# Performance work log

Hardware: AMD Instinct MI355X
Metric: run time of the kernel (lower is better)

The kernel has to match this reference:

```python
import jax, jax.numpy as jnp
import numpy as np

N = 50000          # nodes
E = 400000         # edges (before self loops)
F_IN = 256         # num_node_features
H = 4              # heads
C = 64             # hidden_channels
G = 128            # graphs in batch
NEG_SLOPE = 0.2    # PyG GATConv default


def gat_conv(x, W, att_src, att_dst, bias, src, dst):
    """PyG GATConv (concat=True, add_self_loops=True). x:[N,Fin] -> [N,H*C]."""
    h = (x @ W).reshape(N, H, C)                       # [N,H,C]
    a_src = jnp.einsum('nhc,hc->nh', h, att_src)       # [N,H]
    a_dst = jnp.einsum('nhc,hc->nh', h, att_dst)       # [N,H]
    # add self loops
    loop = jnp.arange(N, dtype=src.dtype)
    s = jnp.concatenate([src, loop])                   # [E+N]
    d = jnp.concatenate([dst, loop])                   # [E+N]
    logits = jax.nn.leaky_relu(a_src[s] + a_dst[d], NEG_SLOPE)  # [E+N,H]
    # segment softmax over destination nodes
    m = jax.ops.segment_max(logits, d, num_segments=N)           # [N,H]
    m = jnp.where(jnp.isneginf(m), 0.0, m)
    ex = jnp.exp(logits - m[d])                                  # [E+N,H]
    denom = jax.ops.segment_sum(ex, d, num_segments=N)           # [N,H]
    alpha = ex / (denom[d] + 1e-16)                              # [E+N,H]
    # weighted scatter-add of source features
    msg = alpha[:, :, None] * h[s]                               # [E+N,H,C]
    out = jax.ops.segment_sum(msg, d, num_segments=N)            # [N,H,C]
    return out.reshape(N, H * C) + bias


def setup_inputs() -> dict:
    key = jax.random.key(0)
    ks = jax.random.split(key, 16)
    HC = H * C
    x = jax.random.normal(ks[0], (N, F_IN), dtype=jnp.float32)
    edge_index = jax.random.randint(ks[1], (2, E), 0, N, dtype=jnp.int32)
    batch = jnp.sort(jax.random.randint(ks[2], (N,), 0, G, dtype=jnp.int32))
    def glorot(k, shape):
        fan = shape[0] + shape[-1]
        return jax.random.uniform(k, shape, jnp.float32, -1.0, 1.0) * np.sqrt(6.0 / fan)
    return {
        'x': x, 'edge_index': edge_index, 'batch': batch,
        'W1': glorot(ks[3], (F_IN, HC)),
        'att_src1': glorot(ks[4], (H, C)), 'att_dst1': glorot(ks[5], (H, C)),
        'b1': jnp.zeros((HC,), jnp.float32),
        'W2': glorot(ks[6], (HC, HC)),
        'att_src2': glorot(ks[7], (H, C)), 'att_dst2': glorot(ks[8], (H, C)),
        'b2': jnp.zeros((HC,), jnp.float32),
        'lin1_w': glorot(ks[9], (HC, HC // 2)), 'lin1_b': jnp.zeros((HC // 2,), jnp.float32),
        'lin2_w': glorot(ks[10], (HC // 2, 2)), 'lin2_b': jnp.zeros((2,), jnp.float32),
    }


def reference(x, edge_index, batch, W1, att_src1, att_dst1, b1,
              W2, att_src2, att_dst2, b2, lin1_w, lin1_b, lin2_w, lin2_b):
    src, dst = edge_index[0], edge_index[1]
    # dropout layers are identity in eval mode
    h = gat_conv(x, W1, att_src1, att_dst1, b1, src, dst)
    h = jax.nn.elu(h)
    h = gat_conv(h, W2, att_src2, att_dst2, b2, src, dst)
    h = jax.nn.elu(h)
    pooled = jax.ops.segment_max(h, batch, num_segments=G)   # [G, H*C]
    pooled = jnp.where(jnp.isneginf(pooled), 0.0, pooled)    # guard empty graphs
    z = pooled @ lin1_w + lin1_b
    z = z @ lin2_w + lin2_b
    return z  # [G, num_classes]
```

## Files before the change

kernel.cpp:

```cpp
#include <hip/hip_runtime.h>
#include <math.h>

#define LRELU_SLOPE 0.2f
#define NEG_INF __int_as_float(0xff800000)

typedef float f32x4 __attribute__((ext_vector_type(4)));
typedef _Float16 f16x8 __attribute__((ext_vector_type(8)));
typedef _Float16 f16x2 __attribute__((ext_vector_type(2)));
typedef unsigned short us8 __attribute__((ext_vector_type(8)));

__device__ __forceinline__ void atomicMaxF(float* addr, float v) {
  if (v >= 0.f) atomicMax((int*)addr, __float_as_int(v));
  else atomicMin((unsigned int*)addr, (unsigned int)__float_as_int(v));
}

__device__ __forceinline__ unsigned short f2h(float f) {
  _Float16 h = (_Float16)f;
  return __builtin_bit_cast(unsigned short, h);
}
__device__ __forceinline__ float h2f(unsigned short u) {
  return (float)__builtin_bit_cast(_Float16, u);
}
__device__ __forceinline__ float2 up2(unsigned int u) {
  f16x2 h = __builtin_bit_cast(f16x2, u);
  return make_float2((float)h.x, (float)h.y);
}

__device__ __forceinline__ void async_copy16(const unsigned short* g, unsigned short* l) {
  __builtin_amdgcn_global_load_lds(
      (const __attribute__((address_space(1))) void*)g,
      (__attribute__((address_space(3))) void*)l, 16, 0, 0);
}

__global__ void conv_w(const float* __restrict__ W1, const float* __restrict__ W2,
                       unsigned short* __restrict__ t1, unsigned short* __restrict__ t2) {
  const float* W = blockIdx.y ? W2 : W1;
  unsigned short* t = blockIdx.y ? t2 : t1;
  int k = blockIdx.x, n = threadIdx.x;
  t[n * 256 + k] = f2h(W[k * 256 + n]);
}

__global__ __launch_bounds__(256) void conv_x(
    const float* __restrict__ x, unsigned short* __restrict__ xo, int total) {
  int base = (blockIdx.x * 256 + threadIdx.x) * 4;
  if (base >= total) return;
  float4 v = *(const float4*)(x + base);
  ushort4 h;
  h.x = f2h(v.x); h.y = f2h(v.y); h.z = f2h(v.z); h.w = f2h(v.w);
  *(ushort4*)(xo + base) = h;
}

__global__ __launch_bounds__(256) void gemm_mfma(
    const unsigned short* __restrict__ A, const unsigned short* __restrict__ Bt,
    unsigned short* __restrict__ C, int M) {
  __shared__ __align__(16) unsigned short sA[128 * 64];
  __shared__ __align__(16) unsigned short sB[128 * 64];
  const int tid = threadIdx.x;
  const int lane = tid & 63;
  const int wave = tid >> 6;
  const int wr = wave >> 1, wc = wave & 1;
  const int bm = blockIdx.x * 128;
  const int bn = blockIdx.y * 128;

  const int srow = lane >> 3;
  const int scol = (((lane & 7) ^ (lane >> 3)) << 3);

  f32x4 acc[4][4];
#pragma unroll
  for (int i = 0; i < 4; ++i)
#pragma unroll
    for (int j = 0; j < 4; ++j) acc[i][j] = (f32x4){0.f, 0.f, 0.f, 0.f};

  for (int kc = 0; kc < 256; kc += 64) {
#pragma unroll
    for (int i = 0; i < 4; ++i) {
      const int r0 = wave * 32 + i * 8;
      const size_t ga = (size_t)(bm + r0 + srow) * 256 + kc + scol;
      const size_t gb = (size_t)(bn + r0 + srow) * 256 + kc + scol;
      async_copy16(A + ga, &sA[r0 * 64]);
      async_copy16(Bt + gb, &sB[r0 * 64]);
    }
    __syncthreads();
#pragma unroll
    for (int ks = 0; ks < 64; ks += 32) {
      const int kbase = ks + ((lane >> 4) << 3);
      const int kx = kbase ^ ((lane & 7) << 3);
      f16x8 af[4], bf[4];
#pragma unroll
      for (int f = 0; f < 4; ++f) {
        int ar = wr * 64 + f * 16 + (lane & 15);
        int br = wc * 64 + f * 16 + (lane & 15);
        af[f] = __builtin_bit_cast(f16x8, *(const us8*)&sA[ar * 64 + kx]);
        bf[f] = __builtin_bit_cast(f16x8, *(const us8*)&sB[br * 64 + kx]);
      }
#pragma unroll
      for (int i = 0; i < 4; ++i)
#pragma unroll
        for (int j = 0; j < 4; ++j)
          acc[i][j] = __builtin_amdgcn_mfma_f32_16x16x32_f16(af[i], bf[j], acc[i][j], 0, 0, 0);
    }
    __syncthreads();
  }
#pragma unroll
  for (int i = 0; i < 4; ++i) {
#pragma unroll
    for (int r = 0; r < 4; ++r) {
      int row = bm + wr * 64 + i * 16 + ((lane >> 4) << 2) + r;
      if (row < M) {
#pragma unroll
        for (int j = 0; j < 4; ++j)
          C[(size_t)row * 256 + bn + wc * 64 + j * 16 + (lane & 15)] = f2h(acc[i][j][r]);
      }
    }
  }
}

__global__ __launch_bounds__(256) void attn_ab(
    const unsigned short* __restrict__ h, const float* __restrict__ att_s,
    const float* __restrict__ att_d, float* __restrict__ a_s,
    float* __restrict__ a_d, int N_) {
  const int slot = threadIdx.x >> 7;
  const int k = threadIdx.x & 127;
  const int head = k >> 5;
  const int c2 = k & 31;
  const float2 ws2 = *(const float2*)(att_s + head * 64 + c2 * 2);
  const float2 wd2 = *(const float2*)(att_d + head * 64 + c2 * 2);
  int n0 = blockIdx.x * 16 + slot * 8;
  int n1 = min(n0 + 8, N_);
  for (int n = n0; n < n1; ++n) {
    unsigned int w = *(const unsigned int*)(h + (size_t)n * 256 + head * 64 + c2 * 2);
    float2 xv = up2(w);
    float ps = xv.x * ws2.x + xv.y * ws2.y;
    float pd = xv.x * wd2.x + xv.y * wd2.y;
#pragma unroll
    for (int off = 16; off > 0; off >>= 1) {
      ps += __shfl_xor(ps, off);
      pd += __shfl_xor(pd, off);
    }
    if (c2 == 0) { a_s[n * 4 + head] = ps; a_d[n * 4 + head] = pd; }
  }
}

__global__ void init_misc(int* __restrict__ count, float* __restrict__ pooled,
                          int N_, int G_) {
  int t = blockIdx.x * 256 + threadIdx.x;
  if (t < N_) count[t] = 1;
  if (t < G_ * 256) pooled[t] = NEG_INF;
}

__global__ void hist_k(const int* __restrict__ dst, int* __restrict__ count, int E_) {
  int t = blockIdx.x * 256 + threadIdx.x;
  if (t < E_) atomicAdd(&count[dst[t]], 1);
}

#define SCB 1024

__global__ __launch_bounds__(256) void scan_phaseA(
    const int* __restrict__ count, int* __restrict__ bsum, int N_) {
  int t = threadIdx.x;
  int base = blockIdx.x * SCB + t * 4;
  int s = 0;
  if (base + 3 < N_) {
    int4 v = *(const int4*)(count + base);
    s = v.x + v.y + v.z + v.w;
  } else {
#pragma unroll
    for (int k = 0; k < 4; ++k) if (base + k < N_) s += count[base + k];
  }
#pragma unroll
  for (int off = 32; off > 0; off >>= 1) s += __shfl_xor(s, off);
  __shared__ int red[4];
  int wave = t >> 6, lane = t & 63;
  if (lane == 0) red[wave] = s;
  __syncthreads();
  if (t == 0) bsum[blockIdx.x] = red[0] + red[1] + red[2] + red[3];
}

__global__ __launch_bounds__(256) void scan_phaseB(
    const int* __restrict__ bsum, int* __restrict__ boff, int nb) {
  __shared__ int tmp[256];
  int t = threadIdx.x;
  int v = (t < nb) ? bsum[t] : 0;
  tmp[t] = v;
  __syncthreads();
  for (int off = 1; off < 256; off <<= 1) {
    int u = (t >= off) ? tmp[t - off] : 0;
    __syncthreads();
    tmp[t] += u;
    __syncthreads();
  }
  if (t < nb) boff[t] = tmp[t] - v;
  if (t == 0) boff[nb] = tmp[255];
}

__global__ __launch_bounds__(256) void scan_phaseC(
    const int* __restrict__ count, const int* __restrict__ boff,
    int* __restrict__ rowptr, int* __restrict__ nxt, int N_, int nb) {
  __shared__ int tmp[256];
  int t = threadIdx.x;
  int base = blockIdx.x * SCB + t * 4;
  int4 v = make_int4(0, 0, 0, 0);
  if (base + 3 < N_) {
    v = *(const int4*)(count + base);
  } else {
    if (base + 0 < N_) v.x = count[base + 0];
    if (base + 1 < N_) v.y = count[base + 1];
    if (base + 2 < N_) v.z = count[base + 2];
  }
  int s = v.x + v.y + v.z + v.w;
  tmp[t] = s;
  __syncthreads();
  for (int off = 1; off < 256; off <<= 1) {
    int u = (t >= off) ? tmp[t - off] : 0;
    __syncthreads();
    tmp[t] += u;
    __syncthreads();
  }
  int run = boff[blockIdx.x] + tmp[t] - s;
  int4 rp;
  rp.x = run; run += v.x;
  rp.y = run; run += v.y;
  rp.z = run; run += v.z;
  rp.w = run;
  if (base + 3 < N_) {
    *(int4*)(rowptr + base) = rp;
    *(int4*)(nxt + base) = rp;
  } else {
    if (base + 0 < N_) { rowptr[base + 0] = rp.x; nxt[base + 0] = rp.x; }
    if (base + 1 < N_) { rowptr[base + 1] = rp.y; nxt[base + 1] = rp.y; }
    if (base + 2 < N_) { rowptr[base + 2] = rp.z; nxt[base + 2] = rp.z; }
  }
  if (blockIdx.x == 0 && t == 0) rowptr[N_] = boff[nb];
}

__global__ void scatter_k(const int* __restrict__ src, const int* __restrict__ dst,
                          int* __restrict__ nxt, int* __restrict__ colx,
                          int* __restrict__ rowx, int E_, int N_) {
  int t = blockIdx.x * 256 + threadIdx.x;
  if (t >= E_ + N_) return;
  int s = (t < E_) ? src[t] : (t - E_);
  int d = (t < E_) ? dst[t] : (t - E_);
  int pos = atomicAdd(&nxt[d], 1);
  colx[pos] = s;
  rowx[pos] = d;
}

__global__ __launch_bounds__(256) void edge_w(
    const int* __restrict__ colx, const int* __restrict__ rowx,
    const float* __restrict__ a_s, const float* __restrict__ a_d,
    float* __restrict__ ew, int T) {
  int t = blockIdx.x * 256 + threadIdx.x;
  if (t >= T) return;
  int s = colx[t], d = rowx[t];
  float4 as4 = *(const float4*)(a_s + (size_t)s * 4);
  float4 ad4 = *(const float4*)(a_d + (size_t)d * 4);
  float l;
  float4 w;
  l = as4.x + ad4.x; l = l > 0.f ? l : LRELU_SLOPE * l; w.x = __expf(l);
  l = as4.y + ad4.y; l = l > 0.f ? l : LRELU_SLOPE * l; w.y = __expf(l);
  l = as4.z + ad4.z; l = l > 0.f ? l : LRELU_SLOPE * l; w.z = __expf(l);
  l = as4.w + ad4.w; l = l > 0.f ? l : LRELU_SLOPE * l; w.w = __expf(l);
  *(float4*)(ew + (size_t)t * 4) = w;
}

__global__ __launch_bounds__(256) void agg(
    const unsigned short* __restrict__ h, const int* __restrict__ rowptr,
    const int* __restrict__ colx, const float* __restrict__ ew,
    const float* __restrict__ bias, unsigned short* __restrict__ out, int N_) {
  const int wave = threadIdx.x >> 6;
  const int lane = threadIdx.x & 63;
  const int n = blockIdx.x * 4 + wave;
  if (n >= N_) return;
  const int head = lane >> 4;
  const size_t coff = (size_t)lane * 4;
  const int e0 = rowptr[n], e1 = rowptr[n + 1];
  float4 acc = make_float4(0.f, 0.f, 0.f, 0.f);
  float dsum = 0.f;
  int j = e0;
  for (; j + 4 <= e1; j += 4) {
    int s0 = colx[j + 0], s1 = colx[j + 1], s2 = colx[j + 2], s3 = colx[j + 3];
    float w0 = ew[(size_t)(j + 0) * 4 + head];
    float w1 = ew[(size_t)(j + 1) * 4 + head];
    float w2 = ew[(size_t)(j + 2) * 4 + head];
    float w3 = ew[(size_t)(j + 3) * 4 + head];
    uint2 g0 = *(const uint2*)(h + (size_t)s0 * 256 + coff);
    uint2 g1 = *(const uint2*)(h + (size_t)s1 * 256 + coff);
    uint2 g2 = *(const uint2*)(h + (size_t)s2 * 256 + coff);
    uint2 g3 = *(const uint2*)(h + (size_t)s3 * 256 + coff);
    dsum += (w0 + w1) + (w2 + w3);
    float2 a0 = up2(g0.x), b0 = up2(g0.y);
    float2 a1 = up2(g1.x), b1 = up2(g1.y);
    float2 a2 = up2(g2.x), b2 = up2(g2.y);
    float2 a3 = up2(g3.x), b3 = up2(g3.y);
    acc.x = fmaf(w0, a0.x, acc.x); acc.y = fmaf(w0, a0.y, acc.y);
    acc.z = fmaf(w0, b0.x, acc.z); acc.w = fmaf(w0, b0.y, acc.w);
    acc.x = fmaf(w1, a1.x, acc.x); acc.y = fmaf(w1, a1.y, acc.y);
    acc.z = fmaf(w1, b1.x, acc.z); acc.w = fmaf(w1, b1.y, acc.w);
    acc.x = fmaf(w2, a2.x, acc.x); acc.y = fmaf(w2, a2.y, acc.y);
    acc.z = fmaf(w2, b2.x, acc.z); acc.w = fmaf(w2, b2.y, acc.w);
    acc.x = fmaf(w3, a3.x, acc.x); acc.y = fmaf(w3, a3.y, acc.y);
    acc.z = fmaf(w3, b3.x, acc.z); acc.w = fmaf(w3, b3.y, acc.w);
  }
  for (; j < e1; ++j) {
    int s = colx[j];
    float w = ew[(size_t)j * 4 + head];
    uint2 g = *(const uint2*)(h + (size_t)s * 256 + coff);
    dsum += w;
    float2 a = up2(g.x), b = up2(g.y);
    acc.x = fmaf(w, a.x, acc.x); acc.y = fmaf(w, a.y, acc.y);
    acc.z = fmaf(w, b.x, acc.z); acc.w = fmaf(w, b.y, acc.w);
  }
  const float inv = 1.f / (dsum + 1e-16f);
  const float4 b4 = *(const float4*)(bias + coff);
  float v;
  float4 o;
  v = acc.x * inv + b4.x; o.x = v > 0.f ? v : expm1f(v);
  v = acc.y * inv + b4.y; o.y = v > 0.f ? v : expm1f(v);
  v = acc.z * inv + b4.z; o.z = v > 0.f ? v : expm1f(v);
  v = acc.w * inv + b4.w; o.w = v > 0.f ? v : expm1f(v);
  ushort4 oh;
  oh.x = f2h(o.x); oh.y = f2h(o.y); oh.z = f2h(o.z); oh.w = f2h(o.w);
  *(ushort4*)(out + (size_t)n * 256 + coff) = oh;
}

#define PNB 32
__global__ __launch_bounds__(256) void pool_max(
    const unsigned short* __restrict__ fb, const int* __restrict__ batch,
    float* __restrict__ pooled, int N_) {
  const int c2 = threadIdx.x & 127;
  const int slot = threadIdx.x >> 7;
  const int ns = blockIdx.x * PNB + slot * 16;
  const int ne = min(ns + 16, N_);
  if (ns >= N_) return;
  float r0 = NEG_INF, r1 = NEG_INF;
  int g = batch[ns];
#pragma unroll 4
  for (int n = ns; n < ne; ++n) {
    int gn = batch[n];
    unsigned int w = *(const unsigned int*)(fb + (size_t)n * 256 + c2 * 2);
    if (gn != g) {
      atomicMaxF(&pooled[(size_t)g * 256 + c2 * 2], r0);
      atomicMaxF(&pooled[(size_t)g * 256 + c2 * 2 + 1], r1);
      r0 = r1 = NEG_INF; g = gn;
    }
    float2 xv = up2(w);
    r0 = fmaxf(r0, xv.x);
    r1 = fmaxf(r1, xv.y);
  }
  atomicMaxF(&pooled[(size_t)g * 256 + c2 * 2], r0);
  atomicMaxF(&pooled[(size_t)g * 256 + c2 * 2 + 1], r1);
}

__global__ __launch_bounds__(128) void head_k(
    const float* __restrict__ pooled, const float* __restrict__ w1,
    const float* __restrict__ b1, const float* __restrict__ w2,
    const float* __restrict__ b2, float* __restrict__ out) {
  __shared__ float ps[256];
  __shared__ float z1[128];
  int g = blockIdx.x;
  int t = threadIdx.x;
  for (int i = t; i < 256; i += 128) {
    float v = pooled[(size_t)g * 256 + i];
    if (v < -1e37f) v = 0.f;
    ps[i] = v;
  }
  __syncthreads();
  float a = b1[t];
  for (int k = 0; k < 256; ++k) a = fmaf(ps[k], w1[k * 128 + t], a);
  z1[t] = a;
  __syncthreads();
  if (t < 2) {
    float a2 = b2[t];
    for (int j = 0; j < 128; ++j) a2 = fmaf(z1[j], w2[j * 2 + t], a2);
    out[g * 2 + t] = a2;
  }
}

extern "C" void kernel_launch(void* const* d_in, const int* in_sizes, int n_in,
                              void* d_out, int out_size, void* d_ws, size_t ws_size,
                              hipStream_t stream) {
  const int N = in_sizes[2];
  const int E = in_sizes[1] / 2;
  const int G = out_size / 2;
  const int T = E + N;
  const int Npad = ((N + 127) / 128) * 128;

  const float* x     = (const float*)d_in[0];
  const int*   ei    = (const int*)d_in[1];
  const int*   src   = ei;
  const int*   dst   = ei + E;
  const int*   batch = (const int*)d_in[2];
  const float* W1    = (const float*)d_in[3];
  const float* atts1 = (const float*)d_in[4];
  const float* attd1 = (const float*)d_in[5];
  const float* b1    = (const float*)d_in[6];
  const float* W2    = (const float*)d_in[7];
  const float* atts2 = (const float*)d_in[8];
  const float* attd2 = (const float*)d_in[9];
  const float* b2    = (const float*)d_in[10];
  const float* l1w   = (const float*)d_in[11];
  const float* l1b   = (const float*)d_in[12];
  const float* l2w   = (const float*)d_in[13];
  const float* l2b   = (const float*)d_in[14];

  uintptr_t p = (uintptr_t)d_ws;
  auto alloc = [&](size_t bytes) -> void* {
    p = (p + 255) & ~(uintptr_t)255;
    void* r = (void*)p;
    p += bytes;
    return r;
  };
  const int nb = (N + SCB - 1) / SCB;
  unsigned short* hbuf = (unsigned short*)alloc((size_t)N * 256 * 2);
  unsigned short* xbuf = (unsigned short*)alloc((size_t)Npad * 256 * 2);
  unsigned short* fbuf = (unsigned short*)alloc((size_t)Npad * 256 * 2);
  float* a_s    = (float*)alloc((size_t)N * 4 * 4);
  float* a_d    = (float*)alloc((size_t)N * 4 * 4);
  float* pooled = (float*)alloc((size_t)G * 256 * 4);
  int*   count  = (int*)alloc((size_t)N * 4);
  int*   rowptr = (int*)alloc((size_t)(N + 1) * 4);
  int*   nxt    = (int*)alloc((size_t)N * 4);
  int*   colx   = (int*)alloc((size_t)T * 4);
  int*   rowx   = (int*)alloc((size_t)T * 4);
  float* ew     = (float*)alloc((size_t)T * 4 * 4);
  int*   bsum   = (int*)alloc((size_t)nb * 4);
  int*   boff   = (int*)alloc((size_t)(nb + 1) * 4);
  unsigned short* wt1 = (unsigned short*)alloc(256 * 256 * 2);
  unsigned short* wt2 = (unsigned short*)alloc(256 * 256 * 2);

  dim3 blk(256);
  dim3 gemmGrid(Npad / 128, 2);
  int initRange = max(N, G * 256);
  int xtot = N * 256;

  conv_w<<<dim3(256, 2), blk, 0, stream>>>(W1, W2, wt1, wt2);
  conv_x<<<(xtot / 4 + 255) / 256, blk, 0, stream>>>(x, xbuf, xtot);
  init_misc<<<(initRange + 255) / 256, blk, 0, stream>>>(count, pooled, N, G);
  hist_k<<<(E + 255) / 256, blk, 0, stream>>>(dst, count, E);
  scan_phaseA<<<nb, blk, 0, stream>>>(count, bsum, N);
  scan_phaseB<<<1, blk, 0, stream>>>(bsum, boff, nb);
  scan_phaseC<<<nb, blk, 0, stream>>>(count, boff, rowptr, nxt, N, nb);
  scatter_k<<<(T + 255) / 256, blk, 0, stream>>>(src, dst, nxt, colx, rowx, E, N);

  gemm_mfma<<<gemmGrid, blk, 0, stream>>>(xbuf, wt1, hbuf, N);
  attn_ab<<<(N + 15) / 16, blk, 0, stream>>>(hbuf, atts1, attd1, a_s, a_d, N);
  edge_w<<<(T + 255) / 256, blk, 0, stream>>>(colx, rowx, a_s, a_d, ew, T);
  agg<<<(N + 3) / 4, blk, 0, stream>>>(hbuf, rowptr, colx, ew, b1, fbuf, N);

  gemm_mfma<<<gemmGrid, blk, 0, stream>>>(fbuf, wt2, hbuf, N);
  attn_ab<<<(N + 15) / 16, blk, 0, stream>>>(hbuf, atts2, attd2, a_s, a_d, N);
  edge_w<<<(T + 255) / 256, blk, 0, stream>>>(colx, rowx, a_s, a_d, ew, T);
  agg<<<(N + 3) / 4, blk, 0, stream>>>(hbuf, rowptr, colx, ew, b2, fbuf, N);

  pool_max<<<(N + PNB - 1) / PNB, blk, 0, stream>>>(fbuf, batch, pooled, N);
  head_k<<<G, 128, 0, stream>>>(pooled, l1w, l1b, l2w, l2b, (float*)d_out);
}
```

Baseline: 256.4 us.

## Fuse attention logit projection into GEMM epilogue and unroll aggregation by eight

Computes the per-node source and destination attention scores inside the MFMA GEMM epilogue, working from the fp32 accumulators with a 16-lane shuffle reduction. This removes the separate attn_ab kernel and its re-read of the fp16 feature matrix, two launches in total. Separately, the aggregation inner loop is unrolled from 4 to 8 edges so more gather loads are in flight per wave. The scores now come from fp32 rather than fp16-rounded values, which changes numerics slightly, and the wider unroll increases register pressure in agg.

```diff
diff --git a/kernel.cpp b/kernel.cpp
--- a/kernel.cpp
+++ b/kernel.cpp
@@ -17,9 +17,6 @@
 __device__ __forceinline__ unsigned short f2h(float f) {
   _Float16 h = (_Float16)f;
   return __builtin_bit_cast(unsigned short, h);
-}
-__device__ __forceinline__ float h2f(unsigned short u) {
-  return (float)__builtin_bit_cast(_Float16, u);
 }
 __device__ __forceinline__ float2 up2(unsigned int u) {
   f16x2 h = __builtin_bit_cast(f16x2, u);
@@ -52,7 +49,9 @@
 
 __global__ __launch_bounds__(256) void gemm_mfma(
     const unsigned short* __restrict__ A, const unsigned short* __restrict__ Bt,
-    unsigned short* __restrict__ C, int M) {
+    const float* __restrict__ att_s, const float* __restrict__ att_d,
+    unsigned short* __restrict__ C, float* __restrict__ a_s,
+    float* __restrict__ a_d, int M) {
   __shared__ __align__(16) unsigned short sA[128 * 64];
   __shared__ __align__(16) unsigned short sB[128 * 64];
   const int tid = threadIdx.x;
@@ -101,6 +100,37 @@
     }
     __syncthreads();
   }
+
+  const int head = blockIdx.y * 2 + wc;
+  float ws[4], wd[4];
+#pragma unroll
+  for (int j = 0; j < 4; ++j) {
+    ws[j] = att_s[head * 64 + j * 16 + (lane & 15)];
+    wd[j] = att_d[head * 64 + j * 16 + (lane & 15)];
+  }
+#pragma unroll
+  for (int i = 0; i < 4; ++i) {
+#pragma unroll
+    for (int r = 0; r < 4; ++r) {
+      float ps = 0.f, pd = 0.f;
+#pragma unroll
+      for (int j = 0; j < 4; ++j) {
+        ps = fmaf(acc[i][j][r], ws[j], ps);
+        pd = fmaf(acc[i][j][r], wd[j], pd);
+      }
+#pragma unroll
+      for (int off = 1; off < 16; off <<= 1) {
+        ps += __shfl_xor(ps, off);
+        pd += __shfl_xor(pd, off);
+      }
+      int row = bm + wr * 64 + i * 16 + ((lane >> 4) << 2) + r;
+      if ((lane & 15) == 0 && row < M) {
+        a_s[row * 4 + head] = ps;
+        a_d[row * 4 + head] = pd;
+      }
+    }
+  }
+
 #pragma unroll
   for (int i = 0; i < 4; ++i) {
 #pragma unroll
@@ -112,32 +142,6 @@
           C[(size_t)row * 256 + bn + wc * 64 + j * 16 + (lane & 15)] = f2h(acc[i][j][r]);
       }
     }
-  }
-}
-
-__global__ __launch_bounds__(256) void attn_ab(
-    const unsigned short* __restrict__ h, const float* __restrict__ att_s,
-    const float* __restrict__ att_d, float* __restrict__ a_s,
-    float* __restrict__ a_d, int N_) {
-  const int slot = threadIdx.x >> 7;
-  const int k = threadIdx.x & 127;
-  const int head = k >> 5;
-  const int c2 = k & 31;
-  const float2 ws2 = *(const float2*)(att_s + head * 64 + c2 * 2);
-  const float2 wd2 = *(const float2*)(att_d + head * 64 + c2 * 2);
-  int n0 = blockIdx.x * 16 + slot * 8;
-  int n1 = min(n0 + 8, N_);
-  for (int n = n0; n < n1; ++n) {
-    unsigned int w = *(const unsigned int*)(h + (size_t)n * 256 + head * 64 + c2 * 2);
-    float2 xv = up2(w);
-    float ps = xv.x * ws2.x + xv.y * ws2.y;
-    float pd = xv.x * wd2.x + xv.y * wd2.y;
-#pragma unroll
-    for (int off = 16; off > 0; off >>= 1) {
-      ps += __shfl_xor(ps, off);
-      pd += __shfl_xor(pd, off);
-    }
-    if (c2 == 0) { a_s[n * 4 + head] = ps; a_d[n * 4 + head] = pd; }
   }
 }
 
@@ -277,29 +281,23 @@
   float4 acc = make_float4(0.f, 0.f, 0.f, 0.f);
   float dsum = 0.f;
   int j = e0;
-  for (; j + 4 <= e1; j += 4) {
-    int s0 = colx[j + 0], s1 = colx[j + 1], s2 = colx[j + 2], s3 = colx[j + 3];
-    float w0 = ew[(size_t)(j + 0) * 4 + head];
-    float w1 = ew[(size_t)(j + 1) * 4 + head];
-    float w2 = ew[(size_t)(j + 2) * 4 + head];
-    float w3 = ew[(size_t)(j + 3) * 4 + head];
-    uint2 g0 = *(const uint2*)(h + (size_t)s0 * 256 + coff);
-    uint2 g1 = *(const uint2*)(h + (size_t)s1 * 256 + coff);
-    uint2 g2 = *(const uint2*)(h + (size_t)s2 * 256 + coff);
-    uint2 g3 = *(const uint2*)(h + (size_t)s3 * 256 + coff);
-    dsum += (w0 + w1) + (w2 + w3);
-    float2 a0 = up2(g0.x), b0 = up2(g0.y);
-    float2 a1 = up2(g1.x), b1 = up2(g1.y);
-    float2 a2 = up2(g2.x), b2 = up2(g2.y);
-    float2 a3 = up2(g3.x), b3 = up2(g3.y);
-    acc.x = fmaf(w0, a0.x, acc.x); acc.y = fmaf(w0, a0.y, acc.y);
-    acc.z = fmaf(w0, b0.x, acc.z); acc.w = fmaf(w0, b0.y, acc.w);
-    acc.x = fmaf(w1, a1.x, acc.x); acc.y = fmaf(w1, a1.y, acc.y);
-    acc.z = fmaf(w1, b1.x, acc.z); acc.w = fmaf(w1, b1.y, acc.w);
-    acc.x = fmaf(w2, a2.x, acc.x); acc.y = fmaf(w2, a2.y, acc.y);
-    acc.z = fmaf(w2, b2.x, acc.z); acc.w = fmaf(w2, b2.y, acc.w);
-    acc.x = fmaf(w3, a3.x, acc.x); acc.y = fmaf(w3, a3.y, acc.y);
-    acc.z = fmaf(w3, b3.x, acc.z); acc.w = fmaf(w3, b3.y, acc.w);
+  for (; j + 8 <= e1; j += 8) {
+    int sx[8];
+    float wv[8];
+    uint2 gv[8];
+#pragma unroll
+    for (int u = 0; u < 8; ++u) sx[u] = colx[j + u];
+#pragma unroll
+    for (int u = 0; u < 8; ++u) wv[u] = ew[(size_t)(j + u) * 4 + head];
+#pragma unroll
+    for (int u = 0; u < 8; ++u) gv[u] = *(const uint2*)(h + (size_t)sx[u] * 256 + coff);
+#pragma unroll
+    for (int u = 0; u < 8; ++u) {
+      dsum += wv[u];
+      float2 a = up2(gv[u].x), b = up2(gv[u].y);
+      acc.x = fmaf(wv[u], a.x, acc.x); acc.y = fmaf(wv[u], a.y, acc.y);
+      acc.z = fmaf(wv[u], b.x, acc.z); acc.w = fmaf(wv[u], b.y, acc.w);
+    }
   }
   for (; j < e1; ++j) {
     int s = colx[j];
@@ -442,13 +440,11 @@
   scan_phaseC<<<nb, blk, 0, stream>>>(count, boff, rowptr, nxt, N, nb);
   scatter_k<<<(T + 255) / 256, blk, 0, stream>>>(src, dst, nxt, colx, rowx, E, N);
 
-  gemm_mfma<<<gemmGrid, blk, 0, stream>>>(xbuf, wt1, hbuf, N);
-  attn_ab<<<(N + 15) / 16, blk, 0, stream>>>(hbuf, atts1, attd1, a_s, a_d, N);
+  gemm_mfma<<<gemmGrid, blk, 0, stream>>>(xbuf, wt1, atts1, attd1, hbuf, a_s, a_d, N);
   edge_w<<<(T + 255) / 256, blk, 0, stream>>>(colx, rowx, a_s, a_d, ew, T);
   agg<<<(N + 3) / 4, blk, 0, stream>>>(hbuf, rowptr, colx, ew, b1, fbuf, N);
 
-  gemm_mfma<<<gemmGrid, blk, 0, stream>>>(fbuf, wt2, hbuf, N);
-  attn_ab<<<(N + 15) / 16, blk, 0, stream>>>(hbuf, atts2, attd2, a_s, a_d, N);
+  gemm_mfma<<<gemmGrid, blk, 0, stream>>>(fbuf, wt2, atts2, attd2, hbuf, a_s, a_d, N);
   edge_w<<<(T + 255) / 256, blk, 0, stream>>>(colx, rowx, a_s, a_d, ew, T);
   agg<<<(N + 3) / 4, blk, 0, stream>>>(hbuf, rowptr, colx, ew, b2, fbuf, N);
 
```

After: 245.4 us. -4.3%, faster.
